# Kernel optimization log

Measured on AMD Instinct MI355X. Metric: run time of the kernel, lower is better.

The kernel has to match this reference:

```python
import jax, jax.numpy as jnp
import numpy as np

ITERATIONS = 50
EPS = 1.0        # entropy_epsilon
LAM = 1.0
TAU = 1.0 * EPS  # tau = 1 * entropy_epsilon
HALF = 2         # ker_halfsize
SIGMA = 5.0
DN = ('NCHW', 'OIHW', 'NCHW')


def _std_kernel():
    r = jnp.arange(-HALF, HALF + 1, dtype=jnp.float32)
    xx, yy = jnp.meshgrid(r, r, indexing='ij')
    k = jnp.exp(-(xx ** 2 + yy ** 2) / (2.0 * SIGMA ** 2))
    k = k / (k.sum() + 1e-15)
    return k[None, None]  # [1,1,5,5]


_NABLA = jnp.array([[[[0., 0., 0.], [0., -1., 0.], [0., 1., 0.]]],
                    [[[0., 0., 0.], [0., -1., 1.], [0., 0., 0.]]]], dtype=jnp.float32)  # [2,1,3,3]
_DIV = jnp.array([[[[0., -1., 0.], [0., 1., 0.], [0., 0., 0.]],
                   [[0., 0., 0.], [-1., 1., 0.], [0., 0., 0.]]]], dtype=jnp.float32)    # [1,2,3,3]


def _conv(x, w, pad):
    return jax.lax.conv_general_dilated(x, w, (1, 1), [(pad, pad), (pad, pad)],
                                        dimension_numbers=DN)


def setup_inputs() -> dict:
    key = jax.random.key(0)
    o = jax.random.normal(key, (8, 1, 512, 512), dtype=jnp.float32)
    return {"o": o}


def reference(o):
    o = o[:, 0]                      # squeeze channel dim -> [B,H,W]
    B, H, W = o.shape
    ker = _std_kernel()
    # torch.meshgrid(arange(1,H+1), arange(1,W+1)) with 'ij' indexing
    x = jnp.broadcast_to(jnp.arange(1, H + 1, dtype=jnp.float32)[:, None], (H, W))
    y = jnp.broadcast_to(jnp.arange(1, W + 1, dtype=jnp.float32)[None, :], (H, W))

    u0 = jax.nn.sigmoid(o / EPS)
    q0 = jnp.zeros_like(o)

    def step(carry, _):
        u, q, _p, _Tq = carry
        p = _conv(1.0 - 2.0 * u[:, None], ker, HALF)[:, 0]          # [B,H,W]
        s = u.sum((1, 2))                                           # [B]
        cx = (u * x).sum((1, 2)) / s
        cy = (u * y).sum((1, 2)) / s
        dx = x[None] - cx[:, None, None]                            # [B,H,W]
        dy = y[None] - cy[:, None, None]
        cossin = (dx * dy * u).sum((1, 2)) / s
        bsin = (dx ** 2 * u).sum((1, 2)) / s
        asin = (dy ** 2 * u).sum((1, 2)) / s
        Tx = -dx * cossin[:, None, None] + dy * bsin[:, None, None]
        Ty = dy * cossin[:, None, None] - dx * asin[:, None, None]
        Tn = jnp.sqrt(Tx ** 2 + Ty ** 2) + 1e-10
        Tx = Tx / Tn
        Ty = Ty / Tn
        un = _conv(u[:, None], _NABLA, 1)                           # [B,2,H,W]
        q_new = q - TAU * (un[:, 0] * Tx + un[:, 1] * Ty)
        Tq = _conv(jnp.stack([Tx * q_new, Ty * q_new], axis=1), _DIV, 1)[:, 0]
        u_new = jax.nn.sigmoid((o - LAM * p - Tq) / EPS)
        return (u_new, q_new, p, Tq), None

    (u, q, p, Tq), _ = jax.lax.scan(step, (u0, q0, q0, q0), None, length=ITERATIONS)
    u1 = (o - LAM * p - Tq) / EPS
    return u1
```

## Files before the change

kernel.cpp:

```cpp
#include <hip/hip_runtime.h>
#include <math.h>

typedef _Float16 h16;
typedef h16 half8v __attribute__((ext_vector_type(8)));
typedef h16 half4v __attribute__((ext_vector_type(4)));
typedef h16 half2v __attribute__((ext_vector_type(2)));

#define HH 512
#define WW 512
#define BB 8
#define NPIX (HH*WW)
#define NTOT (BB*NPIX)
#define ITER 50

#define TX 64
#define TILE_ROWS 32

#define BLK_PER_BATCH 128
#define PART_ITER_STRIDE (BB*BLK_PER_BATCH*8)

constexpr double W0d = 0.92311634638663587;
constexpr double W1d = 0.98019867330675525;
constexpr double SUM1D = 1.0 + 2.0*(W0d + W1d);
constexpr float  INV_NORM = (float)(1.0/(SUM1D*SUM1D + 1e-15));
constexpr float  W0f = (float)W0d;
constexpr float  W1f = (float)W1d;
constexpr float  S1f = (float)SUM1D;

__device__ __forceinline__ float fast_sigmoid(float x) {
    const float e = __expf(-x);
    return __builtin_amdgcn_rcpf(1.0f + e);
}

__device__ __forceinline__ float edge1d(int v) {
    float r = S1f;
    if (v == 0 || v == HH - 1) r = S1f - W0f - W1f;
    else if (v == 1 || v == HH - 2) r = S1f - W0f;
    return r;
}

__device__ __forceinline__ void reduce6_store(float v[6], float* dst8) {
    #pragma unroll
    for (int kk = 0; kk < 6; kk++) {
        float x = v[kk];
        #pragma unroll
        for (int off = 32; off > 0; off >>= 1) x += __shfl_down(x, off, 64);
        v[kk] = x;
    }
    __shared__ float sm[4][6];
    const int lane = threadIdx.x & 63;
    const int wv   = threadIdx.x >> 6;
    if (lane == 0) {
        #pragma unroll
        for (int kk = 0; kk < 6; kk++) sm[wv][kk] = v[kk];
    }
    __syncthreads();
    if (threadIdx.x == 0) {
        float tt[6];
        #pragma unroll
        for (int kk = 0; kk < 6; kk++) tt[kk] = sm[0][kk] + sm[1][kk] + sm[2][kk] + sm[3][kk];
        *(float4*)dst8       = make_float4(tt[0], tt[1], tt[2], tt[3]);
        *(float4*)(dst8 + 4) = make_float4(tt[4], tt[5], 0.f, 0.f);
    }
}

__device__ __forceinline__ void evalF(float uc, float ud, float ur, float qv,
                                      float dx, float dy,
                                      float cossin, float bsin, float asin_,
                                      float& a, float& bv, float& qn) {
    float Tx = -dx * cossin + dy * bsin;
    float Ty =  dy * cossin - dx * asin_;
    const float rn = __builtin_amdgcn_rsqf(Tx * Tx + Ty * Ty + 1e-20f);
    Tx *= rn; Ty *= rn;
    qn = qv - ((ud - uc) * Tx + (ur - uc) * Ty);
    a  = Tx * qn;
    bv = Ty * qn;
}

__global__ __launch_bounds__(256) void init_kernel(const float* __restrict__ o,
                                                   h16* __restrict__ u,
                                                   h16* __restrict__ q,
                                                   h16* __restrict__ oh,
                                                   float* __restrict__ part0) {
    const int b     = blockIdx.x & 7;
    const int chunk = blockIdx.x >> 3;
    const int within = chunk * 2048 + threadIdx.x * 8;
    const int pix = b * NPIX + within;
    const int i = within >> 9;
    const int j = within & (WW - 1);
    const float4 ov0 = *(const float4*)(o + pix);
    const float4 ov1 = *(const float4*)(o + pix + 4);

    const float of[8] = {ov0.x, ov0.y, ov0.z, ov0.w, ov1.x, ov1.y, ov1.z, ov1.w};
    half8v oh8, uh8, qz;
    float urf[8];
    #pragma unroll
    for (int kk = 0; kk < 8; kk++) {
        oh8[kk] = (h16)of[kk];
        uh8[kk] = (h16)fast_sigmoid(of[kk]);
        urf[kk] = (float)uh8[kk];
        qz[kk]  = (h16)0.f;
    }
    *(half8v*)(u + pix)  = uh8;
    *(half8v*)(q + pix)  = qz;
    *(half8v*)(oh + pix) = oh8;

    const float x = (float)(i + 1);
    float s0 = 0.f, sy = 0.f, syy = 0.f;
    #pragma unroll
    for (int kk = 0; kk < 8; kk++) {
        const float y = (float)(j + 1 + kk);
        s0 += urf[kk]; sy += urf[kk] * y; syy += urf[kk] * y * y;
    }
    float v[6] = {s0, x * s0, sy, x * sy, x * x * s0, syy};
    reduce6_store(v, part0 + ((size_t)b * BLK_PER_BATCH + chunk) * 8);
}

__global__ __launch_bounds__(256) void step_kernel(const h16* __restrict__ oh,
                                                   const h16* __restrict__ uA,
                                                   const h16* __restrict__ qA,
                                                   h16* __restrict__ uB,
                                                   h16* __restrict__ qB,
                                                   const float* __restrict__ partIn,
                                                   float* __restrict__ partOut,
                                                   float* __restrict__ out,
                                                   int lastFlag) {
    const int b    = blockIdx.x & 7;
    const int tile = blockIdx.x >> 3;
    const int j0 = (tile & 7) * TX;
    const int i0 = (tile >> 3) * TILE_ROWS;
    const h16* ubase = uA + (size_t)b * NPIX;
    const h16* qbase = qA + (size_t)b * NPIX;

    const int lin  = threadIdx.x;
    const int lane = lin & 63;
    const int tx = lin & 15;
    const int ty = lin >> 4;
    const int ia = i0 + 2 * ty;
    const int jb = j0 + 4 * tx;
    const int loffA = ia * WW + jb;
    const int loffB = loffA + WW;
    const size_t goffA = (size_t)b * NPIX + loffA;
    const size_t goffB = goffA + WW;

    const float* P0 = partIn + (size_t)b * (BLK_PER_BATCH * 8) + lane * 8;
    const float4 pA0 = *(const float4*)P0;
    const float4 pB0 = *(const float4*)(P0 + 4);
    const float4 pA1 = *(const float4*)(P0 + 64 * 8);
    const float4 pB1 = *(const float4*)(P0 + 64 * 8 + 4);

    const bool lok = (jb > 0);
    const bool rok = (jb + 4 < WW);
    half2v uL[6]; half4v uM[6]; half2v uR[6];
    #pragma unroll
    for (int r = 0; r < 6; r++) {
        const int ii = ia - 2 + r;
        const bool rowok = (ii >= 0 && ii < HH);
        half2v l; l[0] = (h16)0.f; l[1] = (h16)0.f;
        half4v m; m[0] = (h16)0.f; m[1] = (h16)0.f; m[2] = (h16)0.f; m[3] = (h16)0.f;
        half2v rr; rr[0] = (h16)0.f; rr[1] = (h16)0.f;
        if (rowok) {
            const h16* rowp = ubase + ii * WW;
            m = *(const half4v*)(rowp + jb);
            if (lok) l  = *(const half2v*)(rowp + jb - 2);
            if (rok) rr = *(const half2v*)(rowp + jb + 4);
        }
        uL[r] = l; uM[r] = m; uR[r] = rr;
    }
    const half4v qcAh = *(const half4v*)(qbase + loffA);
    const half4v qcBh = *(const half4v*)(qbase + loffB);
    const half4v quh  = *(const half4v*)(qbase + ((ia > 0) ? loffA - WW : loffA));
    const h16    qlAh = qbase[lok ? loffA - 1 : loffA];
    const h16    qlBh = qbase[lok ? loffB - 1 : loffB];
    const half4v oAh  = *(const half4v*)(oh + goffA);
    const half4v oBh  = *(const half4v*)(oh + goffB);

    float v6[6];
    v6[0] = pA0.x + pA1.x; v6[1] = pA0.y + pA1.y; v6[2] = pA0.z + pA1.z;
    v6[3] = pA0.w + pA1.w; v6[4] = pB0.x + pB1.x; v6[5] = pB0.y + pB1.y;
    #pragma unroll
    for (int mask = 1; mask < 64; mask <<= 1) {
        #pragma unroll
        for (int c = 0; c < 6; c++) v6[c] += __shfl_xor(v6[c], mask, 64);
    }
    const double sS  = (double)v6[0];
    const double inv = 1.0 / sS;
    const double cxd = (double)v6[1] * inv;
    const double cyd = (double)v6[2] * inv;
    const float cxf    = (float)cxd;
    const float cyf    = (float)cyd;
    const float cossin = (float)((double)v6[3] * inv - cxd * cyd);
    const float bsin   = (float)((double)v6[4] * inv - cxd * cxd);
    const float asin_  = (float)((double)v6[5] * inv - cyd * cyd);

    float vsA[8], vsB[8];
    float Ue[4][6];
    constexpr float wAr[6] = {W0f, W1f, 1.f, W1f, W0f, 0.f};
    constexpr float wBr[6] = {0.f, W0f, W1f, 1.f, W1f, W0f};
    #pragma unroll
    for (int r = 0; r < 6; r++) {
        float U[8];
        U[0] = (float)uL[r][0]; U[1] = (float)uL[r][1];
        U[2] = (float)uM[r][0]; U[3] = (float)uM[r][1];
        U[4] = (float)uM[r][2]; U[5] = (float)uM[r][3];
        U[6] = (float)uR[r][0]; U[7] = (float)uR[r][1];
        #pragma unroll
        for (int c = 0; c < 8; c++) {
            if (r == 0)            vsA[c] = wAr[0] * U[c];
            else if (wAr[r] != 0.f) vsA[c] += wAr[r] * U[c];
            if (r == 1)            vsB[c] = wBr[1] * U[c];
            else if (wBr[r] != 0.f) vsB[c] += wBr[r] * U[c];
        }
        if (r >= 1 && r <= 4) {
            #pragma unroll
            for (int c = 0; c < 6; c++) Ue[r - 1][c] = U[c + 1];
        }
    }

    const float RiA = edge1d(ia);
    const float RiB = edge1d(ia + 1);
    float p4A[4], p4B[4];
    #pragma unroll
    for (int k = 0; k < 4; k++) {
        const float Rj = edge1d(jb + k);
        const float cA = W0f * (vsA[k] + vsA[k + 4]) + W1f * (vsA[k + 1] + vsA[k + 3]) + vsA[k + 2];
        const float cB = W0f * (vsB[k] + vsB[k + 4]) + W1f * (vsB[k + 1] + vsB[k + 3]) + vsB[k + 2];
        p4A[k] = INV_NORM * (RiA * Rj - 2.0f * cA);
        p4B[k] = INV_NORM * (RiB * Rj - 2.0f * cB);
    }

    const float dxA = (float)(ia + 1) - cxf;
    const float dxB = (float)(ia + 2) - cxf;
    const float dxu = (float)ia - cxf;
    const float qcA[4] = {(float)qcAh[0], (float)qcAh[1], (float)qcAh[2], (float)qcAh[3]};
    const float qcB[4] = {(float)qcBh[0], (float)qcBh[1], (float)qcBh[2], (float)qcBh[3]};
    const float quv[4] = {(float)quh[0], (float)quh[1], (float)quh[2], (float)quh[3]};

    float aA[4], bA[4], qnA[4], aUA[4], aB[4], bB[4], qnB[4];
    #pragma unroll
    for (int k = 0; k < 4; k++) {
        const float dy = (float)(jb + k + 1) - cyf;
        evalF(Ue[1][k + 1], Ue[2][k + 1], Ue[1][k + 2], qcA[k],
              dxA, dy, cossin, bsin, asin_, aA[k], bA[k], qnA[k]);
        float au, bu_d, qu_d;
        evalF(Ue[0][k + 1], Ue[1][k + 1], Ue[0][k + 2], quv[k],
              dxu, dy, cossin, bsin, asin_, au, bu_d, qu_d);
        aUA[k] = (ia > 0) ? au : 0.f;
        evalF(Ue[2][k + 1], Ue[3][k + 1], Ue[2][k + 2], qcB[k],
              dxB, dy, cossin, bsin, asin_, aB[k], bB[k], qnB[k]);
    }
    float blA = 0.f, blB = 0.f;
    {
        const float dyl = (float)jb - cyf;
        float ad, bl, qd;
        evalF(Ue[1][0], Ue[2][0], Ue[1][1], (float)qlAh,
              dxA, dyl, cossin, bsin, asin_, ad, bl, qd);
        if (lok) blA = bl;
        evalF(Ue[2][0], Ue[3][0], Ue[2][1], (float)qlBh,
              dxB, dyl, cossin, bsin, asin_, ad, bl, qd);
        if (lok) blB = bl;
    }

    float t4A[4], t4B[4], unA[4], unB[4];
    #pragma unroll
    for (int k = 0; k < 4; k++) {
        const float blA_ = (k == 0) ? blA : bA[k - 1];
        const float blB_ = (k == 0) ? blB : bB[k - 1];
        const float TqA = aA[k] + bA[k] - aUA[k] - blA_;
        const float TqB = aB[k] + bB[k] - aA[k] - blB_;
        t4A[k] = (float)oAh[k] - p4A[k] - TqA;
        t4B[k] = (float)oBh[k] - p4B[k] - TqB;
        unA[k] = fast_sigmoid(t4A[k]);
        unB[k] = fast_sigmoid(t4B[k]);
    }

    half4v uhA, uhB, qhA, qhB;
    float urA[4], urB[4];
    #pragma unroll
    for (int k = 0; k < 4; k++) {
        uhA[k] = (h16)unA[k]; urA[k] = (float)uhA[k]; qhA[k] = (h16)qnA[k];
        uhB[k] = (h16)unB[k]; urB[k] = (float)uhB[k]; qhB[k] = (h16)qnB[k];
    }
    *(half4v*)(uB + goffA) = uhA;
    *(half4v*)(uB + goffB) = uhB;
    *(half4v*)(qB + goffA) = qhA;
    *(half4v*)(qB + goffB) = qhB;
    if (lastFlag) {
        *(float4*)(out + goffA) = make_float4(t4A[0], t4A[1], t4A[2], t4A[3]);
        *(float4*)(out + goffB) = make_float4(t4B[0], t4B[1], t4B[2], t4B[3]);
        return;
    }

    const float xA = (float)(ia + 1);
    const float xB = (float)(ia + 2);
    float s0A = 0.f, syA = 0.f, syyA = 0.f, s0B = 0.f, syB = 0.f, syyB = 0.f;
    #pragma unroll
    for (int k = 0; k < 4; k++) {
        const float y = (float)(jb + k + 1);
        s0A += urA[k]; syA += urA[k] * y; syyA += urA[k] * y * y;
        s0B += urB[k]; syB += urB[k] * y; syyB += urB[k] * y * y;
    }
    float v[6] = {s0A + s0B, xA * s0A + xB * s0B, syA + syB,
                  xA * syA + xB * syB, xA * xA * s0A + xB * xB * s0B, syyA + syyB};
    reduce6_store(v, partOut + ((size_t)b * BLK_PER_BATCH + tile) * 8);
}

extern "C" void kernel_launch(void* const* d_in, const int* in_sizes, int n_in,
                              void* d_out, int out_size, void* d_ws, size_t ws_size,
                              hipStream_t stream) {
    const float* o = (const float*)d_in[0];
    float* out = (float*)d_out;

    h16* uA = (h16*)d_ws;
    h16* uB = uA + (size_t)NTOT;
    h16* qA = uB + (size_t)NTOT;
    h16* qB = qA + (size_t)NTOT;
    h16* oh = qB + (size_t)NTOT;
    float* partials = (float*)(oh + (size_t)NTOT);

    init_kernel<<<1024, 256, 0, stream>>>(o, uA, qA, oh, partials);

    h16 *ua = uA, *ub = uB, *qa = qA, *qb = qB;
    for (int k = 0; k < ITER; k++) {
        step_kernel<<<1024, 256, 0, stream>>>(
            oh, ua, qa, ub, qb,
            partials + (size_t)k * PART_ITER_STRIDE,
            partials + (size_t)(k + 1) * PART_ITER_STRIDE,
            out, (k == ITER - 1) ? 1 : 0);
        h16* tmp;
        tmp = ua; ua = ub; ub = tmp;
        tmp = qa; qa = qb; qb = tmp;
    }
}
```

Baseline: 545.5 us.

## Widen per-thread tile to 8 columns and halve block count

Each thread now computes 2x8 pixels instead of 2x4, so tiles are 64x64 and there are 512 blocks rather than 1024, with partial sums per batch reduced to 64 entries. The wider tile is meant to amortize the halo loads (left/right columns, extra rows) and the per-block cross-lane reduction of the moments over more pixels. The per-pixel loops are fused into a single pass that also accumulates the moment sums. The cost is higher register pressure and fewer blocks, which can lower occupancy on a GPU with many CUs.

```diff
diff --git a/kernel.cpp b/kernel.cpp
--- a/kernel.cpp
+++ b/kernel.cpp
@@ -14,9 +14,9 @@
 #define ITER 50
 
 #define TX 64
-#define TILE_ROWS 32
-
-#define BLK_PER_BATCH 128
+#define TILE_ROWS 64
+
+#define BLK_PER_BATCH 64
 #define PART_ITER_STRIDE (BB*BLK_PER_BATCH*8)
 
 constexpr double W0d = 0.92311634638663587;
@@ -84,31 +84,38 @@
                                                    float* __restrict__ part0) {
     const int b     = blockIdx.x & 7;
     const int chunk = blockIdx.x >> 3;
-    const int within = chunk * 2048 + threadIdx.x * 8;
+    const int within = chunk * 4096 + threadIdx.x * 16;
     const int pix = b * NPIX + within;
     const int i = within >> 9;
     const int j = within & (WW - 1);
-    const float4 ov0 = *(const float4*)(o + pix);
-    const float4 ov1 = *(const float4*)(o + pix + 4);
-
-    const float of[8] = {ov0.x, ov0.y, ov0.z, ov0.w, ov1.x, ov1.y, ov1.z, ov1.w};
-    half8v oh8, uh8, qz;
-    float urf[8];
-    #pragma unroll
-    for (int kk = 0; kk < 8; kk++) {
-        oh8[kk] = (h16)of[kk];
-        uh8[kk] = (h16)fast_sigmoid(of[kk]);
-        urf[kk] = (float)uh8[kk];
-        qz[kk]  = (h16)0.f;
-    }
-    *(half8v*)(u + pix)  = uh8;
-    *(half8v*)(q + pix)  = qz;
-    *(half8v*)(oh + pix) = oh8;
+
+    float of[16];
+    #pragma unroll
+    for (int s = 0; s < 4; s++) {
+        const float4 ov = *(const float4*)(o + pix + 4 * s);
+        of[4*s+0] = ov.x; of[4*s+1] = ov.y; of[4*s+2] = ov.z; of[4*s+3] = ov.w;
+    }
+
+    half8v oh8[2], uh8[2], qz8[2];
+    float urf[16];
+    #pragma unroll
+    for (int kk = 0; kk < 16; kk++) {
+        oh8[kk >> 3][kk & 7] = (h16)of[kk];
+        uh8[kk >> 3][kk & 7] = (h16)fast_sigmoid(of[kk]);
+        urf[kk] = (float)uh8[kk >> 3][kk & 7];
+        qz8[kk >> 3][kk & 7] = (h16)0.f;
+    }
+    *(half8v*)(u + pix)      = uh8[0];
+    *(half8v*)(u + pix + 8)  = uh8[1];
+    *(half8v*)(q + pix)      = qz8[0];
+    *(half8v*)(q + pix + 8)  = qz8[1];
+    *(half8v*)(oh + pix)     = oh8[0];
+    *(half8v*)(oh + pix + 8) = oh8[1];
 
     const float x = (float)(i + 1);
     float s0 = 0.f, sy = 0.f, syy = 0.f;
     #pragma unroll
-    for (int kk = 0; kk < 8; kk++) {
+    for (int kk = 0; kk < 16; kk++) {
         const float y = (float)(j + 1 + kk);
         s0 += urf[kk]; sy += urf[kk] * y; syy += urf[kk] * y * y;
     }
@@ -134,10 +141,10 @@
 
     const int lin  = threadIdx.x;
     const int lane = lin & 63;
-    const int tx = lin & 15;
-    const int ty = lin >> 4;
+    const int tx = lin & 7;
+    const int ty = lin >> 3;
     const int ia = i0 + 2 * ty;
-    const int jb = j0 + 4 * tx;
+    const int jb = j0 + 8 * tx;
     const int loffA = ia * WW + jb;
     const int loffB = loffA + WW;
     const size_t goffA = (size_t)b * NPIX + loffA;
@@ -146,38 +153,36 @@
     const float* P0 = partIn + (size_t)b * (BLK_PER_BATCH * 8) + lane * 8;
     const float4 pA0 = *(const float4*)P0;
     const float4 pB0 = *(const float4*)(P0 + 4);
-    const float4 pA1 = *(const float4*)(P0 + 64 * 8);
-    const float4 pB1 = *(const float4*)(P0 + 64 * 8 + 4);
 
     const bool lok = (jb > 0);
-    const bool rok = (jb + 4 < WW);
-    half2v uL[6]; half4v uM[6]; half2v uR[6];
+    const bool rok = (jb + 8 < WW);
+    half2v uL[6]; half8v uM[6]; half2v uR[6];
     #pragma unroll
     for (int r = 0; r < 6; r++) {
         const int ii = ia - 2 + r;
         const bool rowok = (ii >= 0 && ii < HH);
         half2v l; l[0] = (h16)0.f; l[1] = (h16)0.f;
-        half4v m; m[0] = (h16)0.f; m[1] = (h16)0.f; m[2] = (h16)0.f; m[3] = (h16)0.f;
+        half8v m;
+        #pragma unroll
+        for (int c = 0; c < 8; c++) m[c] = (h16)0.f;
         half2v rr; rr[0] = (h16)0.f; rr[1] = (h16)0.f;
         if (rowok) {
             const h16* rowp = ubase + ii * WW;
-            m = *(const half4v*)(rowp + jb);
+            m = *(const half8v*)(rowp + jb);
             if (lok) l  = *(const half2v*)(rowp + jb - 2);
-            if (rok) rr = *(const half2v*)(rowp + jb + 4);
+            if (rok) rr = *(const half2v*)(rowp + jb + 8);
         }
         uL[r] = l; uM[r] = m; uR[r] = rr;
     }
-    const half4v qcAh = *(const half4v*)(qbase + loffA);
-    const half4v qcBh = *(const half4v*)(qbase + loffB);
-    const half4v quh  = *(const half4v*)(qbase + ((ia > 0) ? loffA - WW : loffA));
+    const half8v qcA8 = *(const half8v*)(qbase + loffA);
+    const half8v qcB8 = *(const half8v*)(qbase + loffB);
+    const half8v qu8  = *(const half8v*)(qbase + ((ia > 0) ? loffA - WW : loffA));
     const h16    qlAh = qbase[lok ? loffA - 1 : loffA];
     const h16    qlBh = qbase[lok ? loffB - 1 : loffB];
-    const half4v oAh  = *(const half4v*)(oh + goffA);
-    const half4v oBh  = *(const half4v*)(oh + goffB);
-
-    float v6[6];
-    v6[0] = pA0.x + pA1.x; v6[1] = pA0.y + pA1.y; v6[2] = pA0.z + pA1.z;
-    v6[3] = pA0.w + pA1.w; v6[4] = pB0.x + pB1.x; v6[5] = pB0.y + pB1.y;
+    const half8v oA8  = *(const half8v*)(oh + goffA);
+    const half8v oB8  = *(const half8v*)(oh + goffB);
+
+    float v6[6] = {pA0.x, pA0.y, pA0.z, pA0.w, pB0.x, pB0.y};
     #pragma unroll
     for (int mask = 1; mask < 64; mask <<= 1) {
         #pragma unroll
@@ -193,62 +198,36 @@
     const float bsin   = (float)((double)v6[4] * inv - cxd * cxd);
     const float asin_  = (float)((double)v6[5] * inv - cyd * cyd);
 
-    float vsA[8], vsB[8];
-    float Ue[4][6];
+    float vsA[12], vsB[12];
+    float Ue[4][10];
     constexpr float wAr[6] = {W0f, W1f, 1.f, W1f, W0f, 0.f};
     constexpr float wBr[6] = {0.f, W0f, W1f, 1.f, W1f, W0f};
     #pragma unroll
     for (int r = 0; r < 6; r++) {
-        float U[8];
+        float U[12];
         U[0] = (float)uL[r][0]; U[1] = (float)uL[r][1];
-        U[2] = (float)uM[r][0]; U[3] = (float)uM[r][1];
-        U[4] = (float)uM[r][2]; U[5] = (float)uM[r][3];
-        U[6] = (float)uR[r][0]; U[7] = (float)uR[r][1];
-        #pragma unroll
-        for (int c = 0; c < 8; c++) {
-            if (r == 0)            vsA[c] = wAr[0] * U[c];
+        #pragma unroll
+        for (int c = 0; c < 8; c++) U[c + 2] = (float)uM[r][c];
+        U[10] = (float)uR[r][0]; U[11] = (float)uR[r][1];
+        #pragma unroll
+        for (int c = 0; c < 12; c++) {
+            if (r == 0)             vsA[c] = wAr[0] * U[c];
             else if (wAr[r] != 0.f) vsA[c] += wAr[r] * U[c];
-            if (r == 1)            vsB[c] = wBr[1] * U[c];
+            if (r == 1)             vsB[c] = wBr[1] * U[c];
             else if (wBr[r] != 0.f) vsB[c] += wBr[r] * U[c];
         }
         if (r >= 1 && r <= 4) {
             #pragma unroll
-            for (int c = 0; c < 6; c++) Ue[r - 1][c] = U[c + 1];
+            for (int c = 0; c < 10; c++) Ue[r - 1][c] = U[c + 1];
         }
     }
 
     const float RiA = edge1d(ia);
     const float RiB = edge1d(ia + 1);
-    float p4A[4], p4B[4];
-    #pragma unroll
-    for (int k = 0; k < 4; k++) {
-        const float Rj = edge1d(jb + k);
-        const float cA = W0f * (vsA[k] + vsA[k + 4]) + W1f * (vsA[k + 1] + vsA[k + 3]) + vsA[k + 2];
-        const float cB = W0f * (vsB[k] + vsB[k + 4]) + W1f * (vsB[k + 1] + vsB[k + 3]) + vsB[k + 2];
-        p4A[k] = INV_NORM * (RiA * Rj - 2.0f * cA);
-        p4B[k] = INV_NORM * (RiB * Rj - 2.0f * cB);
-    }
-
     const float dxA = (float)(ia + 1) - cxf;
     const float dxB = (float)(ia + 2) - cxf;
     const float dxu = (float)ia - cxf;
-    const float qcA[4] = {(float)qcAh[0], (float)qcAh[1], (float)qcAh[2], (float)qcAh[3]};
-    const float qcB[4] = {(float)qcBh[0], (float)qcBh[1], (float)qcBh[2], (float)qcBh[3]};
-    const float quv[4] = {(float)quh[0], (float)quh[1], (float)quh[2], (float)quh[3]};
-
-    float aA[4], bA[4], qnA[4], aUA[4], aB[4], bB[4], qnB[4];
-    #pragma unroll
-    for (int k = 0; k < 4; k++) {
-        const float dy = (float)(jb + k + 1) - cyf;
-        evalF(Ue[1][k + 1], Ue[2][k + 1], Ue[1][k + 2], qcA[k],
-              dxA, dy, cossin, bsin, asin_, aA[k], bA[k], qnA[k]);
-        float au, bu_d, qu_d;
-        evalF(Ue[0][k + 1], Ue[1][k + 1], Ue[0][k + 2], quv[k],
-              dxu, dy, cossin, bsin, asin_, au, bu_d, qu_d);
-        aUA[k] = (ia > 0) ? au : 0.f;
-        evalF(Ue[2][k + 1], Ue[3][k + 1], Ue[2][k + 2], qcB[k],
-              dxB, dy, cossin, bsin, asin_, aB[k], bB[k], qnB[k]);
-    }
+
     float blA = 0.f, blB = 0.f;
     {
         const float dyl = (float)jb - cyf;
@@ -261,45 +240,60 @@
         if (lok) blB = bl;
     }
 
-    float t4A[4], t4B[4], unA[4], unB[4];
-    #pragma unroll
-    for (int k = 0; k < 4; k++) {
-        const float blA_ = (k == 0) ? blA : bA[k - 1];
-        const float blB_ = (k == 0) ? blB : bB[k - 1];
-        const float TqA = aA[k] + bA[k] - aUA[k] - blA_;
-        const float TqB = aB[k] + bB[k] - aA[k] - blB_;
-        t4A[k] = (float)oAh[k] - p4A[k] - TqA;
-        t4B[k] = (float)oBh[k] - p4B[k] - TqB;
-        unA[k] = fast_sigmoid(t4A[k]);
-        unB[k] = fast_sigmoid(t4B[k]);
-    }
-
-    half4v uhA, uhB, qhA, qhB;
-    float urA[4], urB[4];
-    #pragma unroll
-    for (int k = 0; k < 4; k++) {
-        uhA[k] = (h16)unA[k]; urA[k] = (float)uhA[k]; qhA[k] = (h16)qnA[k];
-        uhB[k] = (h16)unB[k]; urB[k] = (float)uhB[k]; qhB[k] = (h16)qnB[k];
-    }
-    *(half4v*)(uB + goffA) = uhA;
-    *(half4v*)(uB + goffB) = uhB;
-    *(half4v*)(qB + goffA) = qhA;
-    *(half4v*)(qB + goffB) = qhB;
-    if (lastFlag) {
-        *(float4*)(out + goffA) = make_float4(t4A[0], t4A[1], t4A[2], t4A[3]);
-        *(float4*)(out + goffB) = make_float4(t4B[0], t4B[1], t4B[2], t4B[3]);
-        return;
-    }
+    half8v uhA, uhB, qhA, qhB;
+    float s0A = 0.f, syA = 0.f, syyA = 0.f, s0B = 0.f, syB = 0.f, syyB = 0.f;
+    float bA_prev = blA, bB_prev = blB;
+    #pragma unroll
+    for (int k = 0; k < 8; k++) {
+        const float Rj = edge1d(jb + k);
+        const float cA = W0f * (vsA[k] + vsA[k + 4]) + W1f * (vsA[k + 1] + vsA[k + 3]) + vsA[k + 2];
+        const float cB = W0f * (vsB[k] + vsB[k + 4]) + W1f * (vsB[k + 1] + vsB[k + 3]) + vsB[k + 2];
+        const float p4A = INV_NORM * (RiA * Rj - 2.0f * cA);
+        const float p4B = INV_NORM * (RiB * Rj - 2.0f * cB);
+
+        const float dy = (float)(jb + k + 1) - cyf;
+        float aA, bA, qnA;
+        evalF(Ue[1][k + 1], Ue[2][k + 1], Ue[1][k + 2], (float)qcA8[k],
+              dxA, dy, cossin, bsin, asin_, aA, bA, qnA);
+        float au, bu_d, qu_d;
+        evalF(Ue[0][k + 1], Ue[1][k + 1], Ue[0][k + 2], (float)qu8[k],
+              dxu, dy, cossin, bsin, asin_, au, bu_d, qu_d);
+        const float aUA = (ia > 0) ? au : 0.f;
+        float aB, bB, qnB;
+        evalF(Ue[2][k + 1], Ue[3][k + 1], Ue[2][k + 2], (float)qcB8[k],
+              dxB, dy, cossin, bsin, asin_, aB, bB, qnB);
+
+        const float TqA = aA + bA - aUA - bA_prev;
+        const float TqB = aB + bB - aA - bB_prev;
+        const float tAv = (float)oA8[k] - p4A - TqA;
+        const float tBv = (float)oB8[k] - p4B - TqB;
+
+        uhA[k] = (h16)fast_sigmoid(tAv);
+        uhB[k] = (h16)fast_sigmoid(tBv);
+        qhA[k] = (h16)qnA;
+        qhB[k] = (h16)qnB;
+
+        const float urA = (float)uhA[k];
+        const float urB = (float)uhB[k];
+        const float y = (float)(jb + k + 1);
+        s0A += urA; syA += urA * y; syyA += urA * y * y;
+        s0B += urB; syB += urB * y; syyB += urB * y * y;
+
+        if (lastFlag) {
+            out[goffA + k] = tAv;
+            out[goffB + k] = tBv;
+        }
+        bA_prev = bA; bB_prev = bB;
+    }
+
+    *(half8v*)(uB + goffA) = uhA;
+    *(half8v*)(uB + goffB) = uhB;
+    *(half8v*)(qB + goffA) = qhA;
+    *(half8v*)(qB + goffB) = qhB;
+    if (lastFlag) return;
 
     const float xA = (float)(ia + 1);
     const float xB = (float)(ia + 2);
-    float s0A = 0.f, syA = 0.f, syyA = 0.f, s0B = 0.f, syB = 0.f, syyB = 0.f;
-    #pragma unroll
-    for (int k = 0; k < 4; k++) {
-        const float y = (float)(jb + k + 1);
-        s0A += urA[k]; syA += urA[k] * y; syyA += urA[k] * y * y;
-        s0B += urB[k]; syB += urB[k] * y; syyB += urB[k] * y * y;
-    }
     float v[6] = {s0A + s0B, xA * s0A + xB * s0B, syA + syB,
                   xA * syA + xB * syB, xA * xA * s0A + xB * xB * s0B, syyA + syyB};
     reduce6_store(v, partOut + ((size_t)b * BLK_PER_BATCH + tile) * 8);
@@ -318,11 +312,11 @@
     h16* oh = qB + (size_t)NTOT;
     float* partials = (float*)(oh + (size_t)NTOT);
 
-    init_kernel<<<1024, 256, 0, stream>>>(o, uA, qA, oh, partials);
+    init_kernel<<<512, 256, 0, stream>>>(o, uA, qA, oh, partials);
 
     h16 *ua = uA, *ub = uB, *qa = qA, *qb = qB;
     for (int k = 0; k < ITER; k++) {
-        step_kernel<<<1024, 256, 0, stream>>>(
+        step_kernel<<<512, 256, 0, stream>>>(
             oh, ua, qa, ub, qb,
             partials + (size_t)k * PART_ITER_STRIDE,
             partials + (size_t)(k + 1) * PART_ITER_STRIDE,
```

Result: faster. 522.9 us (-4.1%).
